# Performance work log

Hardware: AMD Instinct MI355X
Metric: run time of the kernel (lower is better)

Reference implementation:

```python
import jax, jax.numpy as jnp
import numpy as np

T, D, E, DE = 50000, 128, 1600000, 3
EPS = 1e-5


def setup_inputs() -> dict:
    key = jax.random.key(0)
    ks = jax.random.split(key, 8)
    H = jax.random.normal(ks[0], (T, D), dtype=jnp.float32)
    edge_index = jax.random.randint(ks[1], (2, E), 0, T, dtype=jnp.int64)
    edge_attr = jax.random.normal(ks[2], (E, DE), dtype=jnp.float32)
    # phi: Linear(D+DE -> D), GELU, Linear(D -> D)
    s1 = 1.0 / np.sqrt(D + DE)
    s2 = 1.0 / np.sqrt(D)
    W1 = jax.random.uniform(ks[3], (D + DE, D), minval=-s1, maxval=s1, dtype=jnp.float32)
    b1 = jax.random.uniform(ks[4], (D,), minval=-s1, maxval=s1, dtype=jnp.float32)
    W2 = jax.random.uniform(ks[5], (D, D), minval=-s2, maxval=s2, dtype=jnp.float32)
    b2 = jax.random.uniform(ks[6], (D,), minval=-s2, maxval=s2, dtype=jnp.float32)
    gamma = jnp.ones((D,), dtype=jnp.float32)
    beta = jnp.zeros((D,), dtype=jnp.float32)
    return {"H": H, "edge_index": edge_index, "edge_attr": edge_attr,
            "W1": W1, "b1": b1, "W2": W2, "b2": b2, "gamma": gamma, "beta": beta}


def reference(H, edge_index, edge_attr, W1, b1, W2, b2, gamma, beta):
    src, dst = edge_index[0], edge_index[1]
    Hj = H[src]                                   # [E, D] gather
    feat = jnp.concatenate([Hj, edge_attr], axis=-1)  # [E, D+DE]
    h = jax.nn.gelu(feat @ W1 + b1, approximate=False)
    m = h @ W2 + b2                               # [E, D] messages
    agg = jax.ops.segment_sum(m, dst, num_segments=H.shape[0])  # scatter-add
    x = H + agg
    mu = jnp.mean(x, axis=-1, keepdims=True)
    var = jnp.mean((x - mu) ** 2, axis=-1, keepdims=True)
    return (x - mu) * jax.lax.rsqrt(var + EPS) * gamma + beta
```

## Files before the change

### kernel.cpp

```cpp
#include <hip/hip_runtime.h>
#include <hip/hip_bf16.h>

typedef unsigned short u16;
typedef unsigned int u32;
typedef __attribute__((ext_vector_type(8))) __bf16 bf16x8;
typedef __attribute__((ext_vector_type(4))) float f32x4;

#define NT 50000
#define NEDGE 1600000
#define GRID 512
#define NWV 8
#define TOTW 4096
#define NBIN 50176

__device__ __forceinline__ u16 f2bf(float f) {
  unsigned x = __float_as_uint(f);
  x += 0x7fffu + ((x >> 16) & 1u);
  return (u16)(x >> 16);
}

__device__ __forceinline__ int swz(int row, int col) {
  return (row << 7) + (col ^ ((row & 7) << 3));
}

__device__ __forceinline__ float gelu(float v) {
  float t = v * (0.797884561f + 0.0356774081f * v * v);
  return v * __builtin_amdgcn_rcpf(1.0f + __expf(-2.0f * t));
}

__device__ __forceinline__ void atomAddF32(float* p, float v) {
#if defined(__has_builtin)
#if __has_builtin(__builtin_amdgcn_global_atomic_fadd_f32)
  __builtin_amdgcn_global_atomic_fadd_f32((__attribute__((address_space(1))) float*)p, v);
  return;
#endif
#endif
  atomicAdd(p, v);
}


__global__ void prep_all(const float* __restrict__ H, u16* __restrict__ Hb,
                         const float* __restrict__ W1, const float* __restrict__ W2,
                         u16* __restrict__ wsw, const float* __restrict__ b1,
                         u16* __restrict__ wx, u32* __restrict__ cnt) {
  int bid = blockIdx.x, tid = threadIdx.x;
  if (bid < 3125) {
    int t = bid * 256 + tid;
    const float4* s = (const float4*)H + (long)t * 2;
    float4 a = s[0], c = s[1];
    int4 pk;
    pk.x = f2bf(a.x) | ((int)f2bf(a.y) << 16);
    pk.y = f2bf(a.z) | ((int)f2bf(a.w) << 16);
    pk.z = f2bf(c.x) | ((int)f2bf(c.y) << 16);
    pk.w = f2bf(c.z) | ((int)f2bf(c.w) << 16);
    ((int4*)Hb)[t] = pk;
  } else if (bid < 3253) {
    int t = (bid - 3125) * 256 + tid;
    int m = t >> 14;
    int p = t & 16383;
    int row = p >> 7;
    int colq = p & 127;
    int k = colq ^ ((row & 7) << 3);
    const float* W = m ? W2 : W1;
    wsw[t] = f2bf(W[k * 128 + row]);
  } else if (bid < 3257) {
    int t = (bid - 3253) * 256 + tid;
    int row = t >> 3, j = t & 7;
    float v = 0.f;
    if (j < 3) v = W1[(128 + j) * 128 + row];
    else if (j == 3) v = b1[row];
    wx[t] = f2bf(v);
  } else {
    int t = (bid - 3257) * 256 + tid;
    if (t < NBIN) cnt[t] = 0;
  }
}

__global__ void copy_h(const float4* __restrict__ H, float4* __restrict__ out) {
  int t = blockIdx.x * 256 + threadIdx.x;
  out[t] = H[t];
}


__global__ void hist_g(const int* __restrict__ ei, u32* __restrict__ cnt) {
  int e = blockIdx.x * 256 + threadIdx.x;
  atomicAdd(&cnt[ei[NEDGE + e]], 1u);
}

__global__ void scan_blk(u32* __restrict__ cnt, u32* __restrict__ btot) {
  __shared__ u32 ls[1024];
  int tid = threadIdx.x;
  int bin = blockIdx.x * 1024 + tid;
  u32 c = cnt[bin];
  ls[tid] = c;
  __syncthreads();
  for (int o = 1; o < 1024; o <<= 1) {
    u32 t = (tid >= o) ? ls[tid - o] : 0u;
    __syncthreads();
    ls[tid] += t;
    __syncthreads();
  }
  cnt[bin] = ls[tid] - c;
  if (tid == 1023) btot[blockIdx.x] = ls[1023];
}

__global__ void scan_btot(u32* __restrict__ btot) {
  if (threadIdx.x == 0) {
    u32 run = 0;
    for (int i = 0; i < 49; ++i) { u32 t = btot[i]; btot[i] = run; run += t; }
  }
}

__global__ void fin_base(const u32* __restrict__ cnt, const u32* __restrict__ btot,
                         u32* __restrict__ base, u32* __restrict__ pos) {
  int bin = blockIdx.x * 256 + threadIdx.x;
  if (bin < NT) {
    u32 v = cnt[bin] + btot[bin >> 10];
    base[bin] = v;
    pos[bin] = v;
  }
  if (bin == NT) base[NT] = NEDGE;
}

__global__ void scatter_g(const int* __restrict__ ei, const float* __restrict__ ea,
                          u32* __restrict__ pos, uint4* __restrict__ rec) {
  int e = blockIdx.x * 256 + threadIdx.x;
  int d = ei[NEDGE + e];
  int s = ei[e];
  float e0 = ea[e * 3 + 0], e1 = ea[e * 3 + 1], e2 = ea[e * 3 + 2];
  u32 p = atomicAdd(&pos[d], 1u);
  rec[p] = make_uint4((u32)s, __float_as_uint(e0), __float_as_uint(e1), __float_as_uint(e2));
}


__launch_bounds__(512, 2)
__global__ void msg_agg(const u16* __restrict__ Hb,
                        const u16* __restrict__ wsw,
                        const u16* __restrict__ wx,
                        const u32* __restrict__ base,
                        const uint4* __restrict__ rec,
                        u16* __restrict__ hsb) {
  __shared__ __align__(16) u16 lw1[16384];
  __shared__ __align__(16) u16 lw1x[128 * 8];

  const int tid = threadIdx.x;
  {
    const int4* g = (const int4*)wsw;
    int4* d1 = (int4*)lw1;
#pragma unroll
    for (int i = 0; i < 4; ++i) { int c = tid + i * 512; d1[c] = g[c]; }
  }
  if (tid < 128) ((int4*)lw1x)[tid] = ((const int4*)wx)[tid];
  __syncthreads();

  const int wv = tid >> 6, lane = tid & 63;
  const int l15 = lane & 15, l4 = lane >> 4;

  const int gid = blockIdx.x * NWV + wv;
  const int d0 = (int)(((long)gid * NT) / TOTW);
  const int d1i = (int)(((long)(gid + 1) * NT) / TOTW);
  const int nd = d1i - d0;

  for (int b = 0; b < nd; ++b) {
    const int start = (int)base[d0 + b];
    const int cnt = (int)base[d0 + b + 1] - start;

    float racc[8][4];
#pragma unroll
    for (int nt = 0; nt < 8; ++nt)
#pragma unroll
      for (int r = 0; r < 4; ++r) racc[nt][r] = 0.f;

    if (cnt > 0) {
      const int ntile = (cnt + 15) >> 4;
      int i0 = (l15 < cnt) ? l15 : cnt - 1;
      uint4 r4c = rec[start + i0];

      for (int t = 0; t < ntile; ++t) {
        int inx = (t + 1) * 16 + l15;
        if (inx >= cnt) inx = cnt - 1;
        uint4 r4n = rec[start + inx];

        bf16x8 bfc[4];
        {
          const u16* hr = Hb + (long)(int)r4c.x * 128;
#pragma unroll
          for (int ks = 0; ks < 4; ++ks)
            bfc[ks] = *(const bf16x8*)(hr + ks * 32 + l4 * 8);
        }
        int4 xb = make_int4(0, 0, 0, 0);
        if (l4 == 0) {
          xb.x = (int)(f2bf(__uint_as_float(r4c.y)) | ((u32)f2bf(__uint_as_float(r4c.z)) << 16));
          xb.y = (int)(f2bf(__uint_as_float(r4c.w)) | 0x3F800000u);
        }
        bf16x8 bfrx = *(bf16x8*)&xb;
        float vm = (t * 16 + l15 < cnt) ? 1.0f : 0.0f;

#pragma unroll
        for (int nt = 0; nt < 8; ++nt) {
          bf16x8 afr[4];
#pragma unroll
          for (int ks = 0; ks < 4; ++ks)
            afr[ks] = *(const bf16x8*)&lw1[swz(nt * 16 + l15, ks * 32 + l4 * 8)];
          bf16x8 afrx = *(const bf16x8*)&lw1x[(nt * 16 + l15) * 8];
          f32x4 acc = (f32x4){0.f, 0.f, 0.f, 0.f};
#pragma unroll
          for (int ks = 0; ks < 4; ++ks)
            acc = __builtin_amdgcn_mfma_f32_16x16x32_bf16(afr[ks], bfc[ks], acc, 0, 0, 0);
          acc = __builtin_amdgcn_mfma_f32_16x16x32_bf16(afrx, bfrx, acc, 0, 0, 0);
#pragma unroll
          for (int r = 0; r < 4; ++r)
            racc[nt][r] += gelu(acc[r]) * vm;
        }
        r4c = r4n;
      }
    }

#pragma unroll
    for (int nt = 0; nt < 8; ++nt)
#pragma unroll
      for (int r = 0; r < 4; ++r) {
        float s = racc[nt][r];
        s += __shfl_xor(s, 1);
        s += __shfl_xor(s, 2);
        s += __shfl_xor(s, 4);
        s += __shfl_xor(s, 8);
        racc[nt][r] = s;
      }

    if (l15 == 0) {
      u16* hrow = hsb + (long)(d0 + b) * 128;
#pragma unroll
      for (int nt = 0; nt < 8; ++nt) {
        int2 hp;
        hp.x = f2bf(racc[nt][0]) | ((int)f2bf(racc[nt][1]) << 16);
        hp.y = f2bf(racc[nt][2]) | ((int)f2bf(racc[nt][3]) << 16);
        *(int2*)&hrow[nt * 16 + l4 * 4] = hp;
      }
    }
  }
}


__launch_bounds__(256)
__global__ void gemm_ln(const u16* __restrict__ hsb,
                        const float* __restrict__ H,
                        const float* __restrict__ b2,
                        const u16* __restrict__ wsw,
                        const u32* __restrict__ base,
                        const float* __restrict__ gamma,
                        const float* __restrict__ beta,
                        float* __restrict__ out) {
  __shared__ __align__(16) u16 lw2[16384];
  const int tid = threadIdx.x;
  {
    const int4* g = (const int4*)wsw + 2048;
    int4* d2 = (int4*)lw2;
#pragma unroll
    for (int i = 0; i < 8; ++i) { int c = tid + i * 256; d2[c] = g[c]; }
  }
  __syncthreads();

  const int wv = tid >> 6, lane = tid & 63;
  const int l15 = lane & 15, l4 = lane >> 4;
  const int r0 = (blockIdx.x * 4 + wv) * 16;

  bf16x8 ha[4];
#pragma unroll
  for (int ks = 0; ks < 4; ++ks)
    ha[ks] = *(const bf16x8*)(hsb + (long)(r0 + l15) * 128 + ks * 32 + l4 * 8);

  float cntr[4];
#pragma unroll
  for (int r = 0; r < 4; ++r) {
    int row = r0 + l4 * 4 + r;
    if (row > NT - 1) row = NT - 1;
    cntr[r] = (float)(base[row + 1] - base[row]);
  }

  float xv[8][4];
#pragma unroll
  for (int nt = 0; nt < 8; ++nt) {
    bf16x8 bfr2[4];
#pragma unroll
    for (int ks = 0; ks < 4; ++ks)
      bfr2[ks] = *(const bf16x8*)&lw2[swz(nt * 16 + l15, ks * 32 + l4 * 8)];
    float b2v = b2[nt * 16 + l15];
    f32x4 acc = (f32x4){0.f, 0.f, 0.f, 0.f};
#pragma unroll
    for (int ks = 0; ks < 4; ++ks)
      acc = __builtin_amdgcn_mfma_f32_16x16x32_bf16(ha[ks], bfr2[ks], acc, 0, 0, 0);
#pragma unroll
    for (int r = 0; r < 4; ++r) {
      int row = r0 + l4 * 4 + r;
      long o = (long)((row < NT) ? row : NT - 1) * 128 + nt * 16 + l15;
      xv[nt][r] = H[o] + acc[r] + cntr[r] * b2v;
    }
  }

  float mu[4], rs[4];
#pragma unroll
  for (int r = 0; r < 4; ++r) {
    float s = 0.f;
#pragma unroll
    for (int nt = 0; nt < 8; ++nt) s += xv[nt][r];
    s += __shfl_xor(s, 1); s += __shfl_xor(s, 2);
    s += __shfl_xor(s, 4); s += __shfl_xor(s, 8);
    mu[r] = s * (1.0f / 128.0f);
    float q = 0.f;
#pragma unroll
    for (int nt = 0; nt < 8; ++nt) {
      float d = xv[nt][r] - mu[r];
      q += d * d;
    }
    q += __shfl_xor(q, 1); q += __shfl_xor(q, 2);
    q += __shfl_xor(q, 4); q += __shfl_xor(q, 8);
    rs[r] = rsqrtf(q * (1.0f / 128.0f) + 1e-5f);
  }

#pragma unroll
  for (int nt = 0; nt < 8; ++nt) {
    int col = nt * 16 + l15;
    float g = gamma[col], bb = beta[col];
#pragma unroll
    for (int r = 0; r < 4; ++r) {
      int row = r0 + l4 * 4 + r;
      if (row < NT)
        out[(long)row * 128 + col] = (xv[nt][r] - mu[r]) * rs[r] * g + bb;
    }
  }
}


template <int BF16H>
__launch_bounds__(256, 1)
__global__ void msg_atomic(const float* __restrict__ H,
                           const u16* __restrict__ Hb,
                           const int* __restrict__ ei,
                           const float* __restrict__ ea,
                           const float* __restrict__ W1,
                           const float* __restrict__ b1,
                           const float* __restrict__ b2,
                           const u16* __restrict__ wsw,
                           float* __restrict__ out) {
  __shared__ __align__(16) u16 lw1[16384];
  __shared__ __align__(16) u16 lw2[16384];
  __shared__ __align__(16) u16 lh[4 * 2048];
  __shared__ __align__(16) float lep[5][128];

  const int tid = threadIdx.x;
  {
    const int4* g = (const int4*)wsw;
    int4* d1 = (int4*)lw1;
    int4* d2 = (int4*)lw2;
#pragma unroll
    for (int i = 0; i < 8; ++i) {
      int c = tid + i * 256;
      d1[c] = g[c];
      d2[c] = g[2048 + c];
    }
  }
  if (tid < 128) {
    lep[0][tid] = b1[tid];
    lep[1][tid] = W1[128 * 128 + tid];
    lep[2][tid] = W1[129 * 128 + tid];
    lep[3][tid] = W1[130 * 128 + tid];
    lep[4][tid] = b2[tid];
  }
  __syncthreads();

  const int wv = tid >> 6, lane = tid & 63;
  const int l15 = lane & 15, l4 = lane >> 4;
  u16* lhw = lh + wv * 2048;
  const int gwid = blockIdx.x * 4 + wv;

  for (int g = gwid; g < NEDGE / 16; g += 4096) {
    const int eb = g * 16;
    int src = ei[eb + l15];
    float ea0 = ea[(eb + l15) * 3 + 0], ea1 = ea[(eb + l15) * 3 + 1], ea2 = ea[(eb + l15) * 3 + 2];

    bf16x8 bfr[4];
    if (BF16H) {
      const u16* hr = Hb + (long)src * 128;
#pragma unroll
      for (int ks = 0; ks < 4; ++ks)
        bfr[ks] = *(const bf16x8*)(hr + ks * 32 + l4 * 8);
    } else {
      const float* hr = H + (long)src * 128;
#pragma unroll
      for (int ks = 0; ks < 4; ++ks) {
        float4 a = *(const float4*)(hr + ks * 32 + l4 * 8);
        float4 c = *(const float4*)(hr + ks * 32 + l4 * 8 + 4);
        int4 pk;
        pk.x = f2bf(a.x) | ((int)f2bf(a.y) << 16);
        pk.y = f2bf(a.z) | ((int)f2bf(a.w) << 16);
        pk.z = f2bf(c.x) | ((int)f2bf(c.y) << 16);
        pk.w = f2bf(c.z) | ((int)f2bf(c.w) << 16);
        bfr[ks] = *(bf16x8*)&pk;
      }
    }

#pragma unroll
    for (int nt = 0; nt < 8; ++nt) {
      bf16x8 afr[4];
#pragma unroll
      for (int ks = 0; ks < 4; ++ks)
        afr[ks] = *(const bf16x8*)&lw1[swz(nt * 16 + l15, ks * 32 + l4 * 8)];
      f32x4 acc = (f32x4){0.f, 0.f, 0.f, 0.f};
#pragma unroll
      for (int ks = 0; ks < 4; ++ks)
        acc = __builtin_amdgcn_mfma_f32_16x16x32_bf16(afr[ks], bfr[ks], acc, 0, 0, 0);
      f32x4 b1v = *(const f32x4*)&lep[0][nt * 16 + l4 * 4];
      f32x4 w0v = *(const f32x4*)&lep[1][nt * 16 + l4 * 4];
      f32x4 w1v = *(const f32x4*)&lep[2][nt * 16 + l4 * 4];
      f32x4 w2v = *(const f32x4*)&lep[3][nt * 16 + l4 * 4];
      float hv[4];
#pragma unroll
      for (int r = 0; r < 4; ++r) {
        float v = acc[r] + b1v[r] + ea0 * w0v[r] + ea1 * w1v[r] + ea2 * w2v[r];
        hv[r] = gelu(v);
      }
      int2 hp;
      hp.x = f2bf(hv[0]) | ((int)f2bf(hv[1]) << 16);
      hp.y = f2bf(hv[2]) | ((int)f2bf(hv[3]) << 16);
      *(int2*)&lhw[swz(l15, nt * 16 + l4 * 4)] = hp;
    }

    asm volatile("" ::: "memory");

    bf16x8 ha[4];
#pragma unroll
    for (int ks = 0; ks < 4; ++ks)
      ha[ks] = *(const bf16x8*)&lhw[swz(l15, ks * 32 + l4 * 8)];
    int drow[4];
#pragma unroll
    for (int r = 0; r < 4; ++r) drow[r] = ei[NEDGE + eb + l4 * 4 + r];

#pragma unroll
    for (int nt = 0; nt < 8; ++nt) {
      bf16x8 bfr2[4];
#pragma unroll
      for (int ks = 0; ks < 4; ++ks)
        bfr2[ks] = *(const bf16x8*)&lw2[swz(nt * 16 + l15, ks * 32 + l4 * 8)];
      float b2v = lep[4][nt * 16 + l15];
      f32x4 acc = (f32x4){0.f, 0.f, 0.f, 0.f};
#pragma unroll
      for (int ks = 0; ks < 4; ++ks)
        acc = __builtin_amdgcn_mfma_f32_16x16x32_bf16(ha[ks], bfr2[ks], acc, 0, 0, 0);
#pragma unroll
      for (int r = 0; r < 4; ++r)
        atomAddF32(out + (long)drow[r] * 128 + nt * 16 + l15, acc[r] + b2v);
    }
  }
}

__global__ void ln_rows(float* __restrict__ out, const float* __restrict__ gamma,
                        const float* __restrict__ beta) {
  int wave = threadIdx.x >> 6, lane = threadIdx.x & 63;
  int row = blockIdx.x * 4 + wave;
  float2 v = *(const float2*)(out + (long)row * 128 + lane * 2);
  float s = v.x + v.y;
#pragma unroll
  for (int off = 32; off; off >>= 1) s += __shfl_xor(s, off);
  float mu = s * (1.0f / 128.0f);
  float dx = v.x - mu, dy = v.y - mu;
  float q = dx * dx + dy * dy;
#pragma unroll
  for (int off = 32; off; off >>= 1) q += __shfl_xor(q, off);
  float rs = rsqrtf(q * (1.0f / 128.0f) + 1e-5f);
  float2 g = *(const float2*)(gamma + lane * 2);
  float2 b = *(const float2*)(beta + lane * 2);
  float2 o;
  o.x = dx * rs * g.x + b.x;
  o.y = dy * rs * g.y + b.y;
  *(float2*)(out + (long)row * 128 + lane * 2) = o;
}

extern "C" void kernel_launch(void* const* d_in, const int* in_sizes, int n_in,
                              void* d_out, int out_size, void* d_ws, size_t ws_size,
                              hipStream_t stream) {
  const float* H   = (const float*)d_in[0];
  const int* ei    = (const int*)d_in[1];
  const float* ea  = (const float*)d_in[2];
  const float* W1  = (const float*)d_in[3];
  const float* b1  = (const float*)d_in[4];
  const float* W2  = (const float*)d_in[5];
  const float* b2  = (const float*)d_in[6];
  const float* gam = (const float*)d_in[7];
  const float* bet = (const float*)d_in[8];
  float* out = (float*)d_out;

  char* ws = (char*)d_ws;
  u16* wsw  = (u16*)ws;
  u16* wx   = (u16*)(ws + 65536);
  u16* Hb   = (u16*)(ws + 67584);
  u32* cnt  = (u32*)(ws + 12867584);
  u32* base = (u32*)(ws + 13068288);
  u32* pos  = (u32*)(ws + 13268304);
  u32* btot = (u32*)(ws + 13468304);
  uint4* rec = (uint4*)(ws + 13468560);
  u16* hsb  = (u16*)(ws + 39068560);
  const size_t NEED_FULL = 51880848;
  const size_t NEED_HB = 12867584;

  if (ws_size >= NEED_FULL) {
    prep_all<<<3453, 256, 0, stream>>>(H, Hb, W1, W2, wsw, b1, wx, cnt);
    hist_g<<<6250, 256, 0, stream>>>(ei, cnt);
    scan_blk<<<49, 1024, 0, stream>>>(cnt, btot);
    scan_btot<<<1, 64, 0, stream>>>(btot);
    fin_base<<<196, 256, 0, stream>>>(cnt, btot, base, pos);
    scatter_g<<<6250, 256, 0, stream>>>(ei, ea, pos, rec);
    msg_agg<<<GRID, 512, 0, stream>>>(Hb, wsw, wx, base, rec, hsb);
    gemm_ln<<<782, 256, 0, stream>>>(hsb, H, b2, wsw, base, gam, bet, out);
  } else if (ws_size >= NEED_HB) {
    prep_all<<<3453, 256, 0, stream>>>(H, Hb, W1, W2, wsw, b1, wx, cnt);
    copy_h<<<6250, 256, 0, stream>>>((const float4*)H, (float4*)out);
    msg_atomic<1><<<1024, 256, 0, stream>>>(H, Hb, ei, ea, W1, b1, b2, wsw, out);
    ln_rows<<<12500, 256, 0, stream>>>(out, gam, bet);
  } else {
    copy_h<<<6250, 256, 0, stream>>>((const float4*)H, (float4*)out);
    msg_atomic<0><<<1024, 256, 0, stream>>>(H, Hb, ei, ea, W1, b1, b2, wsw, out);
    ln_rows<<<12500, 256, 0, stream>>>(out, gam, bet);
  }
}
```

Baseline: 406.2 us.

## Pack edge records to 8 bytes and swap MFMA operands for cheaper reduction

Edge records shrink from 16-byte uint4 (fp32 attrs) to 8-byte uint2 that pack a 16-bit source index with three bf16 attributes. This halves the scatter write and the msg_agg record reads. Invalid lanes now point at a zeroed padding row of Hb instead of using a per-element mask multiply. The MFMA operand order is swapped so each lane's per-destination sum reduces over accumulator registers plus two cross-lane shuffles instead of four, and every lane writes one output element. The 16-bit source index relies on T being below 65536, and GELU of zero contributes nothing for the padded lanes.

```diff
diff --git a/kernel.cpp b/kernel.cpp
--- a/kernel.cpp
+++ b/kernel.cpp
@@ -70,9 +70,11 @@
     if (j < 3) v = W1[(128 + j) * 128 + row];
     else if (j == 3) v = b1[row];
     wx[t] = f2bf(v);
-  } else {
+  } else if (bid < 3453) {
     int t = (bid - 3257) * 256 + tid;
     if (t < NBIN) cnt[t] = 0;
+  } else {
+    if (tid < 16) ((int4*)(Hb + (long)NT * 128))[tid] = make_int4(0, 0, 0, 0);
   }
 }
 
@@ -123,13 +125,14 @@
 }
 
 __global__ void scatter_g(const int* __restrict__ ei, const float* __restrict__ ea,
-                          u32* __restrict__ pos, uint4* __restrict__ rec) {
+                          u32* __restrict__ pos, uint2* __restrict__ rec) {
   int e = blockIdx.x * 256 + threadIdx.x;
   int d = ei[NEDGE + e];
   int s = ei[e];
   float e0 = ea[e * 3 + 0], e1 = ea[e * 3 + 1], e2 = ea[e * 3 + 2];
   u32 p = atomicAdd(&pos[d], 1u);
-  rec[p] = make_uint4((u32)s, __float_as_uint(e0), __float_as_uint(e1), __float_as_uint(e2));
+  rec[p] = make_uint2((u32)s | ((u32)f2bf(e0) << 16),
+                      (u32)f2bf(e1) | ((u32)f2bf(e2) << 16));
 }
 
 
@@ -138,7 +141,7 @@
                         const u16* __restrict__ wsw,
                         const u16* __restrict__ wx,
                         const u32* __restrict__ base,
-                        const uint4* __restrict__ rec,
+                        const uint2* __restrict__ rec,
                         u16* __restrict__ hsb) {
   __shared__ __align__(16) u16 lw1[16384];
   __shared__ __align__(16) u16 lw1x[128 * 8];
@@ -171,73 +174,68 @@
 #pragma unroll
       for (int r = 0; r < 4; ++r) racc[nt][r] = 0.f;
 
-    if (cnt > 0) {
-      const int ntile = (cnt + 15) >> 4;
+    const int ntile = (cnt + 15) >> 4;
+    uint2 r2c = make_uint2(0, 0);
+    if (ntile > 0) {
       int i0 = (l15 < cnt) ? l15 : cnt - 1;
-      uint4 r4c = rec[start + i0];
-
-      for (int t = 0; t < ntile; ++t) {
-        int inx = (t + 1) * 16 + l15;
-        if (inx >= cnt) inx = cnt - 1;
-        uint4 r4n = rec[start + inx];
-
-        bf16x8 bfc[4];
-        {
-          const u16* hr = Hb + (long)(int)r4c.x * 128;
-#pragma unroll
-          for (int ks = 0; ks < 4; ++ks)
-            bfc[ks] = *(const bf16x8*)(hr + ks * 32 + l4 * 8);
-        }
-        int4 xb = make_int4(0, 0, 0, 0);
-        if (l4 == 0) {
-          xb.x = (int)(f2bf(__uint_as_float(r4c.y)) | ((u32)f2bf(__uint_as_float(r4c.z)) << 16));
-          xb.y = (int)(f2bf(__uint_as_float(r4c.w)) | 0x3F800000u);
-        }
-        bf16x8 bfrx = *(bf16x8*)&xb;
-        float vm = (t * 16 + l15 < cnt) ? 1.0f : 0.0f;
-
-#pragma unroll
-        for (int nt = 0; nt < 8; ++nt) {
-          bf16x8 afr[4];
-#pragma unroll
-          for (int ks = 0; ks < 4; ++ks)
-            afr[ks] = *(const bf16x8*)&lw1[swz(nt * 16 + l15, ks * 32 + l4 * 8)];
-          bf16x8 afrx = *(const bf16x8*)&lw1x[(nt * 16 + l15) * 8];
-          f32x4 acc = (f32x4){0.f, 0.f, 0.f, 0.f};
-#pragma unroll
-          for (int ks = 0; ks < 4; ++ks)
-            acc = __builtin_amdgcn_mfma_f32_16x16x32_bf16(afr[ks], bfc[ks], acc, 0, 0, 0);
-          acc = __builtin_amdgcn_mfma_f32_16x16x32_bf16(afrx, bfrx, acc, 0, 0, 0);
-#pragma unroll
-          for (int r = 0; r < 4; ++r)
-            racc[nt][r] += gelu(acc[r]) * vm;
-        }
-        r4c = r4n;
+      r2c = rec[start + i0];
+    }
+
+    for (int t = 0; t < ntile; ++t) {
+      int inx = (t + 1) * 16 + l15;
+      if (inx >= cnt) inx = cnt - 1;
+      uint2 r2n = rec[start + inx];
+
+      const bool valid = (t * 16 + l15) < cnt;
+      int src = valid ? (int)(r2c.x & 0xFFFFu) : NT;
+      u32 x0 = 0u, x1 = 0u;
+      if (l4 == 0 && valid) {
+        x0 = (r2c.x >> 16) | (r2c.y << 16);
+        x1 = (r2c.y >> 16) | 0x3F800000u;
       }
-    }
-
-#pragma unroll
-    for (int nt = 0; nt < 8; ++nt)
-#pragma unroll
-      for (int r = 0; r < 4; ++r) {
-        float s = racc[nt][r];
-        s += __shfl_xor(s, 1);
-        s += __shfl_xor(s, 2);
-        s += __shfl_xor(s, 4);
-        s += __shfl_xor(s, 8);
-        racc[nt][r] = s;
+      int4 xbi = make_int4((int)x0, (int)x1, 0, 0);
+      bf16x8 bfrx = *(bf16x8*)&xbi;
+
+      bf16x8 bfc[4];
+      {
+        const u16* hr = Hb + (long)src * 128;
+#pragma unroll
+        for (int ks = 0; ks < 4; ++ks)
+          bfc[ks] = *(const bf16x8*)(hr + ks * 32 + l4 * 8);
       }
 
-    if (l15 == 0) {
-      u16* hrow = hsb + (long)(d0 + b) * 128;
 #pragma unroll
       for (int nt = 0; nt < 8; ++nt) {
-        int2 hp;
-        hp.x = f2bf(racc[nt][0]) | ((int)f2bf(racc[nt][1]) << 16);
-        hp.y = f2bf(racc[nt][2]) | ((int)f2bf(racc[nt][3]) << 16);
-        *(int2*)&hrow[nt * 16 + l4 * 4] = hp;
+        bf16x8 afr[4];
+#pragma unroll
+        for (int ks = 0; ks < 4; ++ks)
+          afr[ks] = *(const bf16x8*)&lw1[swz(nt * 16 + l15, ks * 32 + l4 * 8)];
+        bf16x8 afrx = *(const bf16x8*)&lw1x[(nt * 16 + l15) * 8];
+        f32x4 acc = (f32x4){0.f, 0.f, 0.f, 0.f};
+#pragma unroll
+        for (int ks = 0; ks < 4; ++ks)
+          acc = __builtin_amdgcn_mfma_f32_16x16x32_bf16(bfc[ks], afr[ks], acc, 0, 0, 0);
+        acc = __builtin_amdgcn_mfma_f32_16x16x32_bf16(bfrx, afrx, acc, 0, 0, 0);
+#pragma unroll
+        for (int r = 0; r < 4; ++r)
+          racc[nt][r] += gelu(acc[r]);
       }
-    }
+      r2c = r2n;
+    }
+
+    float sv[8];
+#pragma unroll
+    for (int nt = 0; nt < 8; ++nt) {
+      float s = racc[nt][0] + racc[nt][1] + racc[nt][2] + racc[nt][3];
+      s += __shfl_xor(s, 16);
+      s += __shfl_xor(s, 32);
+      sv[nt] = s;
+    }
+    float sa = (l4 == 0) ? sv[0] : (l4 == 1) ? sv[1] : (l4 == 2) ? sv[2] : sv[3];
+    float sb = (l4 == 0) ? sv[4] : (l4 == 1) ? sv[5] : (l4 == 2) ? sv[6] : sv[7];
+    u16* hrow = hsb + (long)(d0 + b) * 128;
+    hrow[l4 * 16 + l15] = f2bf(sa);
+    hrow[64 + l4 * 16 + l15] = f2bf(sb);
   }
 }
 
@@ -491,20 +489,20 @@
   float* out = (float*)d_out;
 
   char* ws = (char*)d_ws;
-  u16* wsw  = (u16*)ws;
-  u16* wx   = (u16*)(ws + 65536);
-  u16* Hb   = (u16*)(ws + 67584);
-  u32* cnt  = (u32*)(ws + 12867584);
-  u32* base = (u32*)(ws + 13068288);
-  u32* pos  = (u32*)(ws + 13268304);
-  u32* btot = (u32*)(ws + 13468304);
-  uint4* rec = (uint4*)(ws + 13468560);
-  u16* hsb  = (u16*)(ws + 39068560);
-  const size_t NEED_FULL = 51880848;
-  const size_t NEED_HB = 12867584;
+  u16* wsw   = (u16*)ws;
+  u16* wx    = (u16*)(ws + 65536);
+  u16* Hb    = (u16*)(ws + 67584);
+  u32* cnt   = (u32*)(ws + 12867840);
+  u32* base  = (u32*)(ws + 13068544);
+  u32* pos   = (u32*)(ws + 13268560);
+  u32* btot  = (u32*)(ws + 13468560);
+  uint2* rec = (uint2*)(ws + 13468816);
+  u16* hsb   = (u16*)(ws + 26268816);
+  const size_t NEED_FULL = 39081104;
+  const size_t NEED_HB = 12867840;
 
   if (ws_size >= NEED_FULL) {
-    prep_all<<<3453, 256, 0, stream>>>(H, Hb, W1, W2, wsw, b1, wx, cnt);
+    prep_all<<<3454, 256, 0, stream>>>(H, Hb, W1, W2, wsw, b1, wx, cnt);
     hist_g<<<6250, 256, 0, stream>>>(ei, cnt);
     scan_blk<<<49, 1024, 0, stream>>>(cnt, btot);
     scan_btot<<<1, 64, 0, stream>>>(btot);
@@ -513,7 +511,7 @@
     msg_agg<<<GRID, 512, 0, stream>>>(Hb, wsw, wx, base, rec, hsb);
     gemm_ln<<<782, 256, 0, stream>>>(hsb, H, b2, wsw, base, gam, bet, out);
   } else if (ws_size >= NEED_HB) {
-    prep_all<<<3453, 256, 0, stream>>>(H, Hb, W1, W2, wsw, b1, wx, cnt);
+    prep_all<<<3454, 256, 0, stream>>>(H, Hb, W1, W2, wsw, b1, wx, cnt);
     copy_h<<<6250, 256, 0, stream>>>((const float4*)H, (float4*)out);
     msg_atomic<1><<<1024, 256, 0, stream>>>(H, Hb, ei, ea, W1, b1, b2, wsw, out);
     ln_rows<<<12500, 256, 0, stream>>>(out, gam, bet);
```

After: 359.5 us. 1.13x faster.
